# Kernel optimization log

Measured on AMD Instinct MI355X. Metric: run time of the kernel, lower is better.

## Reference

```python
import jax, jax.numpy as jnp
import numpy as np

EMBED_DIM = 256
NUM_HEADS = 8
HEAD_DIM = EMBED_DIM // NUM_HEADS


def setup_inputs() -> dict:
    key = jax.random.key(0)
    ks = jax.random.split(key, 12)
    B, E, H, W = 8, EMBED_DIM, 32, 32
    inp = {
        "query": jax.random.normal(ks[0], (B, E, H, W), jnp.float32),
        "key": jax.random.normal(ks[1], (B, E, H, W), jnp.float32),
        "value": jax.random.normal(ks[2], (B, E, H, W), jnp.float32),
        "attn_mask": jax.random.normal(ks[3], (H * W, H * W), jnp.float32),
    }
    # 1x1 conv projections == dense [out, in] matrices; xavier_uniform init
    lim = float(np.sqrt(6.0 / (E + E)))
    for i, nm in enumerate(["Wq", "Wk", "Wv", "Wo"]):
        inp[nm] = jax.random.uniform(ks[4 + i], (E, E), jnp.float32, -lim, lim)
    for i, nm in enumerate(["bq", "bk", "bv", "bo"]):
        inp[nm] = jnp.zeros((E,), jnp.float32)
    return inp


def reference(query, key, value, attn_mask, Wq, bq, Wk, bk, Wv, bv, Wo, bo):
    B, E, Th, Tw = query.shape
    _, _, Sh, Sw = key.shape
    T, S = Th * Tw, Sh * Sw
    nh, hd = NUM_HEADS, HEAD_DIM
    scale = hd ** -0.5

    def proj(x, Wm, bm):  # 1x1 conv: [B,E,h,w] -> [B,E,h,w]
        return jnp.einsum('oi,bihw->bohw', Wm, x) + bm[None, :, None, None]

    q = proj(query, Wq, bq).reshape(B * nh, hd, T).transpose(0, 2, 1)  # [BH,T,hd]
    k = proj(key, Wk, bk).reshape(B * nh, hd, S)                        # [BH,hd,S]
    v = proj(value, Wv, bv).reshape(B * nh, hd, S).transpose(0, 2, 1)   # [BH,S,hd]

    # scaled scores + float mask add (mask broadcasts over B*H)
    attn = jnp.einsum('bth,bhs->bts', q * scale, k) + attn_mask[None, :, :]
    attn = jax.nn.softmax(attn, axis=-1)

    out = jnp.einsum('bts,bsh->bth', attn, v)            # [BH,T,hd]
    out = out.transpose(0, 2, 1).reshape(B, E, Th, Tw)   # [B,E,Th,Tw]
    return proj(out, Wo, bo)
```

## Files before the change

### kernel.cpp

```cpp
#include <hip/hip_runtime.h>
#include <hip/hip_bf16.h>

#define EDIM 256
#define TDIM 1024
#define NHEAD 8
#define HDIM 32
#define NBATCH 8
#define NBH 64
#define INV_LN2 1.4426950408889634f
#define SCALE2 (0.17677669529663687f * 1.4426950408889634f)

typedef __attribute__((ext_vector_type(8))) short short8;
typedef __attribute__((ext_vector_type(4))) short short4v;
typedef __attribute__((ext_vector_type(4))) float f32x4;

__device__ __forceinline__ f32x4 mfma16(short8 a, short8 b, f32x4 c) {
  return __builtin_amdgcn_mfma_f32_16x16x32_bf16(a, b, c, 0, 0, 0);
}
__device__ __forceinline__ float bf2f(short h) {
  return __uint_as_float(((unsigned)(unsigned short)h) << 16);
}
__device__ __forceinline__ short f2bf1(float x) {
  unsigned u = __float_as_uint(x);
  u = (u + 0x7fffu + ((u >> 16) & 1u)) >> 16;
  return (short)u;
}
__device__ __forceinline__ short4v packbf4(float a, float b, float c, float d) {
  __hip_bfloat162 x = __float22bfloat162_rn(make_float2(a, b));
  __hip_bfloat162 y = __float22bfloat162_rn(make_float2(c, d));
  unsigned ux, uy;
  __builtin_memcpy(&ux, &x, 4);
  __builtin_memcpy(&uy, &y, 4);
  short4v r;
  r[0] = (short)(ux & 0xffffu); r[1] = (short)(ux >> 16);
  r[2] = (short)(uy & 0xffffu); r[3] = (short)(uy >> 16);
  return r;
}
__device__ __forceinline__ short f2h(float x) {
  _Float16 h = (_Float16)x;
  short s; __builtin_memcpy(&s, &h, 2); return s;
}
__device__ __forceinline__ float h2f(short x) {
  _Float16 h; __builtin_memcpy(&h, &x, 2); return (float)h;
}
__device__ __forceinline__ float fexp2(float x) {
#if __has_builtin(__builtin_amdgcn_exp2f)
  return __builtin_amdgcn_exp2f(x);
#else
  return exp2f(x);
#endif
}

__global__ __launch_bounds__(256) void prepare(
    const float* __restrict__ w0, const float* __restrict__ w1,
    const float* __restrict__ w2, const float* __restrict__ w3,
    const float* __restrict__ mask, const float* __restrict__ qin,
    const float* __restrict__ kin, const float* __restrict__ vin,
    short* __restrict__ wsp, float* __restrict__ maskS,
    short* __restrict__ Xs)
{
  const int blk = blockIdx.x;
  const int tid = threadIdx.x;
  __shared__ float Tl[64][65];

  if (blk < 256) {
    const int z = blk >> 6, chunk = blk & 63;
    const float* W = (z == 0) ? w0 : (z == 1) ? w1 : (z == 2) ? w2 : w3;
    short* hi = wsp + (size_t)z * 2 * EDIM * EDIM;
    short* lo = hi + EDIM * EDIM;
    const int idx = chunk * 1024 + tid * 4;
    float4 v = *(const float4*)&W[idx];
    short4v h = packbf4(v.x, v.y, v.z, v.w);
    short4v l = packbf4(v.x - bf2f(h[0]), v.y - bf2f(h[1]),
                        v.z - bf2f(h[2]), v.w - bf2f(h[3]));
    *(short4v*)&hi[idx] = h;
    *(short4v*)&lo[idx] = l;
  } else if (blk < 512) {
    const int i = blk - 256;
    const int t0 = (i >> 4) * 64, s0 = (i & 15) * 64;
    const int r = tid >> 2, c = (tid & 3) * 16;
#pragma unroll
    for (int g = 0; g < 4; ++g) {
      float4 v = *(const float4*)&mask[(size_t)(t0 + r) * TDIM + s0 + c + 4 * g];
      Tl[c + 4 * g + 0][r] = v.x * INV_LN2;
      Tl[c + 4 * g + 1][r] = v.y * INV_LN2;
      Tl[c + 4 * g + 2][r] = v.z * INV_LN2;
      Tl[c + 4 * g + 3][r] = v.w * INV_LN2;
    }
    __syncthreads();
    const int sql = tid >> 6, tl = tid & 63;
    unsigned short* mS = (unsigned short*)maskS;
#pragma unroll
    for (int g = 0; g < 4; ++g) {
      const int sq = g * 4 + sql;
      short4v o;
      o[0] = f2h(Tl[sq * 4 + 0][tl]);
      o[1] = f2h(Tl[sq * 4 + 1][tl]);
      o[2] = f2h(Tl[sq * 4 + 2][tl]);
      o[3] = f2h(Tl[sq * 4 + 3][tl]);
      *(short4v*)&mS[(size_t)(s0 / 4 + sq) * 4096 + (size_t)(t0 + tl) * 4] = o;
    }
  } else {
    const int bz = blk - 512;
    const int tt = bz & 15, ee = (bz >> 4) & 3, tb = bz >> 6;
    const float* src = ((tb >> 3) == 0) ? qin : ((tb >> 3) == 1) ? kin : vin;
    const int b = tb & 7;
    const int t0 = tt * 64, e0 = ee * 64;
    const float* s = src + (size_t)b * EDIM * TDIM;
    const int tl = tid & 63, er = (tid >> 6) * 16;
#pragma unroll
    for (int i = 0; i < 16; ++i)
      Tl[tl][er + i] = s[(size_t)(e0 + er + i) * TDIM + t0 + tl];
    __syncthreads();
    const int rt = tid >> 2, seg = (tid & 3) * 16;
    float v[16];
#pragma unroll
    for (int i = 0; i < 16; ++i) v[i] = Tl[rt][seg + i];
    short* dst = Xs + ((size_t)tb * TDIM + t0 + rt) * EDIM + e0 + seg;
#pragma unroll
    for (int i = 0; i < 4; ++i)
      *(short4v*)&dst[4 * i] =
          packbf4(v[4 * i], v[4 * i + 1], v[4 * i + 2], v[4 * i + 3]);
  }
}

__global__ __launch_bounds__(256, 4) void proj(
    const short* __restrict__ Xbase, const short* __restrict__ wsp,
    const float* __restrict__ b0, const float* __restrict__ b1,
    const float* __restrict__ b2, const float* __restrict__ b3,
    short* __restrict__ Qt, short* __restrict__ KtHi, short* __restrict__ KtLo,
    short* __restrict__ VHi, float* __restrict__ Of, int tbase)
{
  const int z = blockIdx.z;
  const int tloc = z >> 3;
  const int tensor = tbase + tloc;
  const int batch = z & 7;
  const int m0 = blockIdx.y * 64;
  const int n0 = blockIdx.x * 64;
  const int tid = threadIdx.x;
  const int w = tid >> 6, lane = tid & 63, q = lane >> 4, l16 = lane & 15;

  const float* bias = (tensor == 0) ? b0 : (tensor == 1) ? b1
                      : (tensor == 2) ? b2 : b3;
  const short* Wh = wsp + (size_t)tensor * 2 * EDIM * EDIM;
  const short* Wl = Wh + EDIM * EDIM;
  const short* Xt = Xbase + ((size_t)(tloc * NBATCH + batch) * TDIM + n0) * EDIM;

  __shared__ __align__(16) short Xl[64 * 256];

  short8 ah[8], al[8];
  {
    const short* wrh = Wh + (size_t)(m0 + 16 * w + l16) * EDIM + q * 8;
    const short* wrl = Wl + (size_t)(m0 + 16 * w + l16) * EDIM + q * 8;
#pragma unroll
    for (int c = 0; c < 8; ++c) {
      ah[c] = *(const short8*)&wrh[c * 32];
      al[c] = *(const short8*)&wrl[c * 32];
    }
  }
#pragma unroll
  for (int k2 = 0; k2 < 8; ++k2) {
    const int tl = k2 * 8 + (tid >> 5);
    const int e8 = tid & 31;
    short8 vv = *(const short8*)&Xt[(size_t)k2 * 2048 + tid * 8];
    *(short8*)&Xl[tl * 256 + ((e8 ^ (tl & 7)) << 3)] = vv;
  }
  __syncthreads();

  f32x4 acc[4] = {};
  const int lm = l16 & 7;
#pragma unroll
  for (int c = 0; c < 8; ++c) {
#pragma unroll
    for (int j = 0; j < 4; ++j) {
      short8 bf = *(const short8*)&Xl[(16 * j + l16) * 256 +
                                      (((c * 4 + q) ^ lm) << 3)];
      acc[j] = mfma16(ah[c], bf, acc[j]);
      acc[j] = mfma16(al[c], bf, acc[j]);
    }
  }

  if (tensor == 3) {
#pragma unroll
    for (int j = 0; j < 4; ++j) {
      const int n = n0 + 16 * j + l16;
#pragma unroll
      for (int r = 0; r < 4; ++r) {
        const int m = m0 + 16 * w + 4 * q + r;
        Of[((size_t)batch * EDIM + m) * TDIM + n] = acc[j][r] + bias[m];
      }
    }
    return;
  }
  if (tensor == 2) {
#pragma unroll
    for (int j = 0; j < 4; ++j) {
      const int n = n0 + 16 * j + l16;
#pragma unroll
      for (int r = 0; r < 4; ++r) {
        const int m = m0 + 16 * w + 4 * q + r;
        VHi[((size_t)batch * EDIM + m) * TDIM + n] = f2bf1(acc[j][r] + bias[m]);
      }
    }
    return;
  }
  __syncthreads();
  float (*Lt)[68] = (float (*)[68])Xl;
#pragma unroll
  for (int j = 0; j < 4; ++j) {
    const int mb = m0 + 16 * w + 4 * q;
    float4 v4;
    v4.x = acc[j][0] + bias[mb + 0];
    v4.y = acc[j][1] + bias[mb + 1];
    v4.z = acc[j][2] + bias[mb + 2];
    v4.w = acc[j][3] + bias[mb + 3];
    if (tensor == 0) { v4.x *= SCALE2; v4.y *= SCALE2; v4.z *= SCALE2; v4.w *= SCALE2; }
    *(float4*)&Lt[16 * j + l16][16 * w + 4 * q] = v4;
  }
  __syncthreads();
  {
    const int tl = tid >> 2;
    const int seg = (tid & 3) * 16;
    const int ch = m0 + seg;
    const int bh = batch * NHEAD + (ch >> 5);
    const int d0 = ch & 31;
    const size_t o = ((size_t)bh * TDIM + n0 + tl) * HDIM + d0;
    float v[16];
#pragma unroll
    for (int i = 0; i < 16; ++i) v[i] = Lt[tl][seg + i];
    if (tensor == 0) {
#pragma unroll
      for (int i = 0; i < 4; ++i)
        *(short4v*)&Qt[o + 4 * i] =
            packbf4(v[4 * i], v[4 * i + 1], v[4 * i + 2], v[4 * i + 3]);
    } else {
#pragma unroll
      for (int i = 0; i < 4; ++i) {
        short4v h = packbf4(v[4 * i], v[4 * i + 1], v[4 * i + 2], v[4 * i + 3]);
        short4v l = packbf4(v[4 * i + 0] - bf2f(h[0]), v[4 * i + 1] - bf2f(h[1]),
                            v[4 * i + 2] - bf2f(h[2]), v[4 * i + 3] - bf2f(h[3]));
        *(short4v*)&KtHi[o + 4 * i] = h;
        *(short4v*)&KtLo[o + 4 * i] = l;
      }
    }
  }
}

__global__ __launch_bounds__(256, 3) void flash6(
    const short* __restrict__ Qt, const short* __restrict__ KtHi,
    const short* __restrict__ KtLo, const short* __restrict__ VHi,
    const float* __restrict__ maskS, unsigned short* __restrict__ p0,
    unsigned short* __restrict__ p1, unsigned short* __restrict__ p2,
    unsigned short* __restrict__ p3, float* __restrict__ Lh)
{
  const int tid = threadIdx.x;
  const int w = tid >> 6, lane = tid & 63, q = lane >> 4, l16 = lane & 15;
  const int bh = blockIdx.x;
  const int t0 = blockIdx.y * 128 + w * 32;
  const int quarter = blockIdx.z;
  const int sbase = quarter * 256;

  __shared__ __align__(16) short KhS[8192];
  __shared__ __align__(16) short KlS[8192];
  __shared__ __align__(16) short VS[8192];
  __shared__ __align__(16) short Ps[4][32][72];

  {
    const short* kgh = KtHi + (size_t)bh * TDIM * HDIM + (size_t)sbase * HDIM;
    const short* kgl = KtLo + (size_t)bh * TDIM * HDIM + (size_t)sbase * HDIM;
    const short* vgl = VHi + (size_t)bh * HDIM * TDIM + sbase;
#pragma unroll
    for (int r = 0; r < 4; ++r) {
      *(short8*)&KhS[r * 2048 + tid * 8] =
          *(const short8*)&kgh[r * 2048 + tid * 8];
      *(short8*)&KlS[r * 2048 + tid * 8] =
          *(const short8*)&kgl[r * 2048 + tid * 8];
      const int idx = r * 256 + tid;
      const int d = idx >> 5;
      const int g = idx & 31;
      const int gp = (g & 24) | ((g ^ d) & 7);
      *(short8*)&VS[d * 256 + gp * 8] =
          *(const short8*)&vgl[(size_t)d * TDIM + g * 8];
    }
  }

  const short* qb = Qt + (size_t)bh * TDIM * HDIM;
  const unsigned short* m_p = (const unsigned short*)maskS +
                              ((size_t)(sbase >> 2) + q) * 4096 +
                              (size_t)(t0 + l16) * 4;

  short8 qf0 = *(const short8*)&qb[(size_t)(t0 + l16) * HDIM + q * 8];
  short8 qf1 = *(const short8*)&qb[(size_t)(t0 + 16 + l16) * HDIM + q * 8];

  short4v ma[4][4], mb[4][4];
#pragma unroll
  for (int it = 0; it < 4; ++it) {
    const unsigned short* m_i = m_p + it * 65536;
#pragma unroll
    for (int mt = 0; mt < 4; ++mt) {
      ma[it][mt] = *(const short4v*)(m_i + (size_t)mt * 16384);
      mb[it][mt] = *(const short4v*)(m_i + (size_t)mt * 16384 + 64);
    }
  }
  __builtin_amdgcn_sched_barrier(0);

  __syncthreads();

  float ls[2] = {0.f, 0.f};
  f32x4 oacc[2][2] = {};
  const int vswz = l16 & 7;

#pragma unroll
  for (int it = 0; it < 4; ++it) {
    f32x4 sc[4][2];
#pragma unroll
    for (int mt = 0; mt < 4; ++mt) {
      sc[mt][0] = f32x4{h2f(ma[it][mt][0]), h2f(ma[it][mt][1]),
                        h2f(ma[it][mt][2]), h2f(ma[it][mt][3])};
      sc[mt][1] = f32x4{h2f(mb[it][mt][0]), h2f(mb[it][mt][1]),
                        h2f(mb[it][mt][2]), h2f(mb[it][mt][3])};
    }
#pragma unroll
    for (int mt = 0; mt < 4; ++mt) {
      const int srow = (64 * it + 16 * mt + l16) * 32 + q * 8;
      short8 kh = *(const short8*)&KhS[srow];
      short8 kl = *(const short8*)&KlS[srow];
      sc[mt][0] = mfma16(kh, qf0, sc[mt][0]);
      sc[mt][0] = mfma16(kl, qf0, sc[mt][0]);
      sc[mt][1] = mfma16(kh, qf1, sc[mt][1]);
      sc[mt][1] = mfma16(kl, qf1, sc[mt][1]);
    }
#pragma unroll
    for (int nt = 0; nt < 2; ++nt) {
      float p[16];
#pragma unroll
      for (int mt = 0; mt < 4; ++mt)
#pragma unroll
        for (int r = 0; r < 4; ++r) p[4 * mt + r] = fexp2(sc[mt][nt][r]);
      ls[nt] += (((p[0] + p[1]) + (p[2] + p[3])) +
                 ((p[4] + p[5]) + (p[6] + p[7]))) +
                (((p[8] + p[9]) + (p[10] + p[11])) +
                 ((p[12] + p[13]) + (p[14] + p[15])));
#pragma unroll
      for (int mt = 0; mt < 4; ++mt)
        *(short4v*)&Ps[w][16 * nt + l16][16 * mt + 4 * q] =
            packbf4(p[4 * mt], p[4 * mt + 1], p[4 * mt + 2], p[4 * mt + 3]);
    }
#pragma unroll
    for (int c = 0; c < 2; ++c) {
      short8 pf0 = *(const short8*)&Ps[w][l16][32 * c + 8 * q];
      short8 pf1 = *(const short8*)&Ps[w][16 + l16][32 * c + 8 * q];
#pragma unroll
      for (int dt = 0; dt < 2; ++dt) {
        const int gsw = 8 * it + ((4 * c + q) ^ vswz);
        short8 vh = *(const short8*)&VS[(16 * dt + l16) * 256 + gsw * 8];
        oacc[dt][0] = mfma16(vh, pf0, oacc[dt][0]);
        oacc[dt][1] = mfma16(vh, pf1, oacc[dt][1]);
      }
    }
  }

  ls[0] += __shfl_xor(ls[0], 16);
  ls[0] += __shfl_xor(ls[0], 32);
  ls[1] += __shfl_xor(ls[1], 16);
  ls[1] += __shfl_xor(ls[1], 32);

  unsigned short* Op = (quarter == 0) ? p0 : (quarter == 1) ? p1
                       : (quarter == 2) ? p2 : p3;
#pragma unroll
  for (int nt = 0; nt < 2; ++nt) {
    const int t = t0 + 16 * nt + l16;
#pragma unroll
    for (int dt = 0; dt < 2; ++dt)
#pragma unroll
      for (int r = 0; r < 4; ++r) {
        const int d = 16 * dt + 4 * q + r;
        Op[((size_t)bh * HDIM + d) * TDIM + t] =
            (unsigned short)f2bf1(oacc[dt][nt][r]);
      }
    if (q == 0)
      Lh[(size_t)quarter * NBH * TDIM + (size_t)bh * TDIM + t] = ls[nt];
  }
}

__global__ __launch_bounds__(256) void merge4(
    const unsigned short* __restrict__ p0, const unsigned short* __restrict__ p1,
    const unsigned short* __restrict__ p2, const unsigned short* __restrict__ p3,
    const float* __restrict__ Lh, short* __restrict__ Xm)
{
  const int b = blockIdx.z;
  const int t0 = blockIdx.x * 64;
  const int e0 = blockIdx.y * 64;
  const int tid = threadIdx.x;
  __shared__ float Lt[64][65];

  const int t = t0 + (tid & 63);
  const int eb = e0 + (tid >> 6) * 16;
  const int bh = b * NHEAD + (eb >> 5);
  const size_t mo = (size_t)bh * TDIM + t;
  const float l = Lh[mo] + Lh[65536 + mo] + Lh[131072 + mo] + Lh[196608 + mo];
  const float inv = 1.f / l;

  const size_t ro = ((size_t)b * EDIM + eb) * TDIM + t;
#pragma unroll
  for (int i = 0; i < 16; ++i) {
    const size_t o = ro + (size_t)i * TDIM;
    const float v = (bf2f((short)p0[o]) + bf2f((short)p1[o]) +
                     bf2f((short)p2[o]) + bf2f((short)p3[o])) * inv;
    Lt[tid & 63][(tid >> 6) * 16 + i] = v;
  }
  __syncthreads();
  const int tl = tid >> 2, seg = (tid & 3) * 16;
  float v[16];
#pragma unroll
  for (int i = 0; i < 16; ++i) v[i] = Lt[tl][seg + i];
  short* dst = Xm + ((size_t)b * TDIM + t0 + tl) * EDIM + e0 + seg;
#pragma unroll
  for (int i = 0; i < 4; ++i)
    *(short4v*)&dst[4 * i] =
        packbf4(v[4 * i], v[4 * i + 1], v[4 * i + 2], v[4 * i + 3]);
}

extern "C" void kernel_launch(void* const* d_in, const int* in_sizes, int n_in,
                              void* d_out, int out_size, void* d_ws, size_t ws_size,
                              hipStream_t stream)
{
  const float* query = (const float*)d_in[0];
  const float* key   = (const float*)d_in[1];
  const float* value = (const float*)d_in[2];
  const float* msk   = (const float*)d_in[3];
  const float* Wq = (const float*)d_in[4];
  const float* Wk = (const float*)d_in[5];
  const float* Wv = (const float*)d_in[6];
  const float* Wo = (const float*)d_in[7];
  const float* bq = (const float*)d_in[8];
  const float* bk = (const float*)d_in[9];
  const float* bv = (const float*)d_in[10];
  const float* bo = (const float*)d_in[11];
  float* out = (float*)d_out;

  const size_t PL = (size_t)NBATCH * TDIM * EDIM;
  short* Xs    = (short*)d_ws;
  short* Qt    = Xs + 3 * PL;
  short* KtHi  = Qt + PL;
  short* KtLo  = KtHi + PL;
  short* VHi   = KtLo + PL;
  short* Wsp   = VHi + PL;
  float* maskS = (float*)(Wsp + 4 * 2 * EDIM * EDIM);
  float* Lh    = maskS + (size_t)TDIM * TDIM;
  unsigned short* pp0 = (unsigned short*)Xs;
  unsigned short* pp1 = pp0 + PL;
  unsigned short* pp2 = pp1 + PL;
  unsigned short* pp3 = (unsigned short*)d_out;
  short* Xm = Qt;

  dim3 bb(256);
  hipLaunchKernelGGL(prepare, dim3(2048), bb, 0, stream,
                     Wq, Wk, Wv, Wo, msk, query, key, value, Wsp, maskS, Xs);
  hipLaunchKernelGGL(proj, dim3(16, 4, 24), bb, 0, stream,
                     Xs, Wsp, bq, bk, bv, bo, Qt, KtHi, KtLo, VHi,
                     (float*)nullptr, 0);
  hipLaunchKernelGGL(flash6, dim3(64, 8, 4), bb, 0, stream,
                     Qt, KtHi, KtLo, VHi, maskS, pp0, pp1, pp2, pp3, Lh);
  hipLaunchKernelGGL(merge4, dim3(16, 4, 8), bb, 0, stream,
                     pp0, pp1, pp2, pp3, Lh, Xm);
  hipLaunchKernelGGL(proj, dim3(16, 4, 8), bb, 0, stream,
                     Xm, Wsp, bq, bk, bv, bo, Qt, KtHi, KtLo, VHi, out, 3);
}
```

Baseline: 154.5 us.

## Split K/V shared-memory staging into two halves to shrink LDS footprint

The K-hi, K-lo and V tiles in shared memory are halved. The 256-key quarter is now processed in two 128-key halves, with a block-wide reload of the second half between two barriers. This cuts LDS per block from about 66KB to about 42KB, which could let more blocks reside per CU. The cost is extra __syncthreads and a load stall mid-kernel that is not overlapped with compute.

```diff
diff --git a/kernel.cpp b/kernel.cpp
--- a/kernel.cpp
+++ b/kernel.cpp
@@ -260,27 +260,28 @@
   const int quarter = blockIdx.z;
   const int sbase = quarter * 256;
 
-  __shared__ __align__(16) short KhS[8192];
-  __shared__ __align__(16) short KlS[8192];
-  __shared__ __align__(16) short VS[8192];
+  __shared__ __align__(16) short KhS[4096];
+  __shared__ __align__(16) short KlS[4096];
+  __shared__ __align__(16) short VS[4096];
   __shared__ __align__(16) short Ps[4][32][72];
 
+  const short* kgh_b = KtHi + (size_t)bh * TDIM * HDIM + (size_t)sbase * HDIM;
+  const short* kgl_b = KtLo + (size_t)bh * TDIM * HDIM + (size_t)sbase * HDIM;
+  const short* vgl_b = VHi + (size_t)bh * HDIM * TDIM + sbase;
+
   {
-    const short* kgh = KtHi + (size_t)bh * TDIM * HDIM + (size_t)sbase * HDIM;
-    const short* kgl = KtLo + (size_t)bh * TDIM * HDIM + (size_t)sbase * HDIM;
-    const short* vgl = VHi + (size_t)bh * HDIM * TDIM + sbase;
-#pragma unroll
-    for (int r = 0; r < 4; ++r) {
+#pragma unroll
+    for (int r = 0; r < 2; ++r) {
       *(short8*)&KhS[r * 2048 + tid * 8] =
-          *(const short8*)&kgh[r * 2048 + tid * 8];
+          *(const short8*)&kgh_b[r * 2048 + tid * 8];
       *(short8*)&KlS[r * 2048 + tid * 8] =
-          *(const short8*)&kgl[r * 2048 + tid * 8];
+          *(const short8*)&kgl_b[r * 2048 + tid * 8];
       const int idx = r * 256 + tid;
-      const int d = idx >> 5;
-      const int g = idx & 31;
-      const int gp = (g & 24) | ((g ^ d) & 7);
-      *(short8*)&VS[d * 256 + gp * 8] =
-          *(const short8*)&vgl[(size_t)d * TDIM + g * 8];
+      const int d = idx >> 4;
+      const int g = idx & 15;
+      const int gp = (g & 8) | ((g ^ d) & 7);
+      *(short8*)&VS[d * 128 + gp * 8] =
+          *(const short8*)&vgl_b[(size_t)d * TDIM + g * 8];
     }
   }
 
@@ -311,51 +312,73 @@
   const int vswz = l16 & 7;
 
 #pragma unroll
-  for (int it = 0; it < 4; ++it) {
-    f32x4 sc[4][2];
-#pragma unroll
-    for (int mt = 0; mt < 4; ++mt) {
-      sc[mt][0] = f32x4{h2f(ma[it][mt][0]), h2f(ma[it][mt][1]),
-                        h2f(ma[it][mt][2]), h2f(ma[it][mt][3])};
-      sc[mt][1] = f32x4{h2f(mb[it][mt][0]), h2f(mb[it][mt][1]),
-                        h2f(mb[it][mt][2]), h2f(mb[it][mt][3])};
-    }
-#pragma unroll
-    for (int mt = 0; mt < 4; ++mt) {
-      const int srow = (64 * it + 16 * mt + l16) * 32 + q * 8;
-      short8 kh = *(const short8*)&KhS[srow];
-      short8 kl = *(const short8*)&KlS[srow];
-      sc[mt][0] = mfma16(kh, qf0, sc[mt][0]);
-      sc[mt][0] = mfma16(kl, qf0, sc[mt][0]);
-      sc[mt][1] = mfma16(kh, qf1, sc[mt][1]);
-      sc[mt][1] = mfma16(kl, qf1, sc[mt][1]);
-    }
-#pragma unroll
-    for (int nt = 0; nt < 2; ++nt) {
-      float p[16];
-#pragma unroll
-      for (int mt = 0; mt < 4; ++mt)
-#pragma unroll
-        for (int r = 0; r < 4; ++r) p[4 * mt + r] = fexp2(sc[mt][nt][r]);
-      ls[nt] += (((p[0] + p[1]) + (p[2] + p[3])) +
-                 ((p[4] + p[5]) + (p[6] + p[7]))) +
-                (((p[8] + p[9]) + (p[10] + p[11])) +
-                 ((p[12] + p[13]) + (p[14] + p[15])));
-#pragma unroll
-      for (int mt = 0; mt < 4; ++mt)
-        *(short4v*)&Ps[w][16 * nt + l16][16 * mt + 4 * q] =
-            packbf4(p[4 * mt], p[4 * mt + 1], p[4 * mt + 2], p[4 * mt + 3]);
-    }
-#pragma unroll
-    for (int c = 0; c < 2; ++c) {
-      short8 pf0 = *(const short8*)&Ps[w][l16][32 * c + 8 * q];
-      short8 pf1 = *(const short8*)&Ps[w][16 + l16][32 * c + 8 * q];
-#pragma unroll
-      for (int dt = 0; dt < 2; ++dt) {
-        const int gsw = 8 * it + ((4 * c + q) ^ vswz);
-        short8 vh = *(const short8*)&VS[(16 * dt + l16) * 256 + gsw * 8];
-        oacc[dt][0] = mfma16(vh, pf0, oacc[dt][0]);
-        oacc[dt][1] = mfma16(vh, pf1, oacc[dt][1]);
+  for (int half = 0; half < 2; ++half) {
+    if (half == 1) {
+      __syncthreads();
+#pragma unroll
+      for (int r = 0; r < 2; ++r) {
+        *(short8*)&KhS[r * 2048 + tid * 8] =
+            *(const short8*)&kgh_b[4096 + r * 2048 + tid * 8];
+        *(short8*)&KlS[r * 2048 + tid * 8] =
+            *(const short8*)&kgl_b[4096 + r * 2048 + tid * 8];
+        const int idx = r * 256 + tid;
+        const int d = idx >> 4;
+        const int g = idx & 15;
+        const int gp = (g & 8) | ((g ^ d) & 7);
+        *(short8*)&VS[d * 128 + gp * 8] =
+            *(const short8*)&vgl_b[(size_t)d * TDIM + 128 + g * 8];
+      }
+      __syncthreads();
+    }
+#pragma unroll
+    for (int ih = 0; ih < 2; ++ih) {
+      const int it = half * 2 + ih;
+      f32x4 sc[4][2];
+#pragma unroll
+      for (int mt = 0; mt < 4; ++mt) {
+        sc[mt][0] = f32x4{h2f(ma[it][mt][0]), h2f(ma[it][mt][1]),
+                          h2f(ma[it][mt][2]), h2f(ma[it][mt][3])};
+        sc[mt][1] = f32x4{h2f(mb[it][mt][0]), h2f(mb[it][mt][1]),
+                          h2f(mb[it][mt][2]), h2f(mb[it][mt][3])};
+      }
+#pragma unroll
+      for (int mt = 0; mt < 4; ++mt) {
+        const int srow = (64 * ih + 16 * mt + l16) * 32 + q * 8;
+        short8 kh = *(const short8*)&KhS[srow];
+        short8 kl = *(const short8*)&KlS[srow];
+        sc[mt][0] = mfma16(kh, qf0, sc[mt][0]);
+        sc[mt][0] = mfma16(kl, qf0, sc[mt][0]);
+        sc[mt][1] = mfma16(kh, qf1, sc[mt][1]);
+        sc[mt][1] = mfma16(kl, qf1, sc[mt][1]);
+      }
+#pragma unroll
+      for (int nt = 0; nt < 2; ++nt) {
+        float p[16];
+#pragma unroll
+        for (int mt = 0; mt < 4; ++mt)
+#pragma unroll
+          for (int r = 0; r < 4; ++r) p[4 * mt + r] = fexp2(sc[mt][nt][r]);
+        ls[nt] += (((p[0] + p[1]) + (p[2] + p[3])) +
+                   ((p[4] + p[5]) + (p[6] + p[7]))) +
+                  (((p[8] + p[9]) + (p[10] + p[11])) +
+                   ((p[12] + p[13]) + (p[14] + p[15])));
+#pragma unroll
+        for (int mt = 0; mt < 4; ++mt)
+          *(short4v*)&Ps[w][16 * nt + l16][16 * mt + 4 * q] =
+              packbf4(p[4 * mt], p[4 * mt + 1], p[4 * mt + 2], p[4 * mt + 3]);
+      }
+#pragma unroll
+      for (int c = 0; c < 2; ++c) {
+        short8 pf0 = *(const short8*)&Ps[w][l16][32 * c + 8 * q];
+        short8 pf1 = *(const short8*)&Ps[w][16 + l16][32 * c + 8 * q];
+#pragma unroll
+        for (int dt = 0; dt < 2; ++dt) {
+          const int g = 8 * ih + 4 * c + q;
+          const int gp = (g & 8) | ((g ^ vswz) & 7);
+          short8 vh = *(const short8*)&VS[(16 * dt + l16) * 128 + gp * 8];
+          oacc[dt][0] = mfma16(vh, pf0, oacc[dt][0]);
+          oacc[dt][1] = mfma16(vh, pf1, oacc[dt][1]);
+        }
       }
     }
   }
```

New measurement: 155.7 us. No clear change (+0.8%).
